# Kernel tuning notes

Measured on AMD Instinct MI355X. Metric: run time of the kernel, lower is better.

Reference implementation:

```python
import jax, jax.numpy as jnp
import numpy as np
from jax import lax

B, H, W = 8, 512, 512


def setup_inputs() -> dict:
    key = jax.random.key(0)
    k1, k2, k3, k4, k5 = jax.random.split(key, 5)
    img = jax.random.uniform(k1, (B, 3, H, W), jnp.float32)
    omega = 0.8 + 0.15 * jax.random.uniform(k2, (B, 1), jnp.float32)
    atmospheric_light = 0.5 + 0.5 * jax.random.uniform(k3, (B, 3), jnp.float32)
    L_low = 2.0 * jax.random.uniform(k4, (B, 1), jnp.float32)          # percent in [0,2)
    L_high = 95.0 + 4.0 * jax.random.uniform(k5, (B, 1), jnp.float32)  # percent in [95,99)
    guided_radius = 15  # python int, uniform across batch (original clamps to [1,50])
    return {"img": img, "omega": omega, "atmospheric_light": atmospheric_light,
            "L_low": L_low, "L_high": L_high, "guided_radius": guided_radius}


def _box_filter(x, r):
    # reflect-pad + mean over (2r+1)x(2r+1) window, separable (exactly avg_pool2d on reflect-padded input)
    k = 2 * r + 1
    xp = jnp.pad(x, ((0, 0), (0, 0), (r, r), (r, r)), mode='reflect')
    s = lax.reduce_window(xp, 0.0, lax.add, (1, 1, k, 1), (1, 1, 1, 1), 'VALID')
    s = lax.reduce_window(s, 0.0, lax.add, (1, 1, 1, k), (1, 1, 1, 1), 'VALID')
    return s / (k * k)


def _forward(img, omega, atmospheric_light, L_low, L_high, r):
    eps = 0.5
    Bb, Cc, Hh, Ww = img.shape
    A = atmospheric_light.reshape(Bb, 3, 1, 1)
    # initial transmission: t = 1 - omega * min_c(I/A)
    dark = jnp.min(img / (A + 1e-8), axis=1, keepdims=True)           # (B,1,H,W)
    t0 = 1.0 - omega.reshape(Bb, 1, 1, 1) * dark
    # gradient constraint (weights from t0, applied to shifted copies)
    wx = jnp.exp(-jnp.abs(t0[:, :, :, 1:] - t0[:, :, :, :-1]))
    tx = jnp.concatenate([t0[:, :, :, :1], t0[:, :, :, :-1] * wx], axis=3)
    wy = jnp.exp(-jnp.abs(t0[:, :, 1:, :] - t0[:, :, :-1, :]))
    tg = jnp.concatenate([tx[:, :, :1, :], tx[:, :, :-1, :] * wy], axis=2)
    # guided filter with grayscale guide
    rgb_w = jnp.array([0.299, 0.587, 0.114], dtype=img.dtype).reshape(1, 3, 1, 1)
    gray = jnp.sum(img * rgb_w, axis=1, keepdims=True)                # (B,1,H,W)
    mI = _box_filter(gray, r)
    mp = _box_filter(tg, r)
    mIp = _box_filter(gray * tg, r)
    cov_Ip = mIp - mI * mp
    var_I = _box_filter(gray * gray, r) - mI * mI
    a = cov_Ip / (var_I + eps)
    b = mp - a * mI
    t_final = jnp.clip(_box_filter(a, r) * gray + _box_filter(b, r), 0.1, 1.0)
    # restoration
    J = jnp.clip((img - A) / (t_final + 1e-8) + A, 0.0, 1.0)
    # percentile color stretch (vectorized over B and C)
    n = Hh * Ww
    svals = jnp.sort(J.reshape(Bb, Cc, n), axis=-1)
    li = jnp.clip((L_low / 100.0 * n).astype(jnp.int32), 0, n - 1)    # (B,1)
    hi = jnp.clip((L_high / 100.0 * n).astype(jnp.int32), 0, n - 1)
    p_low = jnp.take_along_axis(svals, jnp.broadcast_to(li[:, :, None], (Bb, Cc, 1)), axis=-1).reshape(Bb, Cc, 1, 1)
    p_high = jnp.take_along_axis(svals, jnp.broadcast_to(hi[:, :, None], (Bb, Cc, 1)), axis=-1).reshape(Bb, Cc, 1, 1)
    out = (jnp.clip(J, p_low, p_high) - p_low) / (p_high - p_low + 1e-8)
    return jnp.clip(out, 0.0, 1.0)


def reference(img, omega, atmospheric_light, L_low, L_high, guided_radius):
    r = max(1, min(int(guided_radius), 50))
    return _forward(img, omega, atmospheric_light, L_low, L_high, r)
```

## Files before the change

### kernel.cpp

```cpp
#include <hip/hip_runtime.h>
#include <cstdint>

constexpr int Bb = 8, Hh = 512, Ww = 512;
constexpr int HWn = Hh * Ww;
constexpr int CH23 = 16;
constexpr int CHK4 = 8;
constexpr int NBIN = 1024;
constexpr int NSUB = 32;

__device__ __forceinline__ int reflect_idx(int p, int n) {
    p = (p < 0) ? -p : p;
    return (p < n) ? p : (2 * n - 2 - p);
}
__device__ __forceinline__ int clamp_r(const int* rad) {
    int r = rad[0];
    return (r < 1) ? 1 : ((r > 50) ? 50 : r);
}

__global__ __launch_bounds__(512) void k1_stats_h(
    const float* __restrict__ img, const float* __restrict__ omega,
    const float* __restrict__ atm, const int* __restrict__ rad,
    float4* __restrict__ hq, unsigned int* __restrict__ histzero)
{
    const int i = blockIdx.x;
    const int b = blockIdx.y;
    const int j = threadIdx.x;
    const int fbid = b * gridDim.x + i;
    if (fbid < 48) histzero[fbid * 512 + j] = 0u;
    const int r = clamp_r(rad);

    __shared__ float t0c[512], t0p[512];
    __shared__ float4 Pb[512];
    __shared__ float4 wsum[8];

    const float om = omega[b];
    const float iA0 = 1.0f / (atm[b*3+0] + 1e-8f);
    const float iA1 = 1.0f / (atm[b*3+1] + 1e-8f);
    const float iA2 = 1.0f / (atm[b*3+2] + 1e-8f);
    const float* imb = img + (size_t)b * 3 * HWn;
    const int ip = (i > 0) ? (i - 1) : 0;

    float r0 = imb[0*HWn + i*Ww + j];
    float g0 = imb[1*HWn + i*Ww + j];
    float b0 = imb[2*HWn + i*Ww + j];
    t0c[j] = 1.0f - om * fminf(fminf(r0*iA0, g0*iA1), b0*iA2);
    float r1 = imb[0*HWn + ip*Ww + j];
    float g1 = imb[1*HWn + ip*Ww + j];
    float b1 = imb[2*HWn + ip*Ww + j];
    t0p[j] = 1.0f - om * fminf(fminf(r1*iA0, g1*iA1), b1*iA2);
    float gr = 0.299f*r0 + 0.587f*g0 + 0.114f*b0;
    __syncthreads();

    float tx = (j == 0) ? t0p[0] : t0p[j-1] * __expf(-fabsf(t0p[j] - t0p[j-1]));
    float tgv = (i == 0) ? tx : tx * __expf(-fabsf(t0c[j] - t0p[j]));

    const int lane = j & 63, wv = j >> 6;
    float4 incl;
    incl.x = gr; incl.y = tgv; incl.z = gr * tgv; incl.w = gr * gr;
    #pragma unroll
    for (int off = 1; off < 64; off <<= 1) {
        float ux = __shfl_up(incl.x, off);
        float uy = __shfl_up(incl.y, off);
        float uz = __shfl_up(incl.z, off);
        float uw = __shfl_up(incl.w, off);
        if (lane >= off) { incl.x += ux; incl.y += uy; incl.z += uz; incl.w += uw; }
    }
    if (lane == 63) wsum[wv] = incl;
    __syncthreads();
    float4 o4; o4.x = 0.f; o4.y = 0.f; o4.z = 0.f; o4.w = 0.f;
    #pragma unroll
    for (int w = 0; w < 7; ++w) {
        if (w < wv) {
            float4 t = wsum[w];
            o4.x += t.x; o4.y += t.y; o4.z += t.z; o4.w += t.w;
        }
    }
    float4 P; P.x = incl.x + o4.x; P.y = incl.y + o4.y; P.z = incl.z + o4.z; P.w = incl.w + o4.w;
    Pb[j] = P;
    __syncthreads();

    const int lo = j - r, hi = j + r;
    float4 s = Pb[(hi > 511) ? 511 : hi];
    if (lo > 0) {
        float4 t = Pb[lo-1];
        s.x -= t.x; s.y -= t.y; s.z -= t.z; s.w -= t.w;
    }
    if (lo < 0) {
        float4 t = Pb[r - j], u = Pb[0];
        s.x += t.x - u.x; s.y += t.y - u.y; s.z += t.z - u.z; s.w += t.w - u.w;
    }
    if (hi > 511) {
        float4 t = Pb[510], u = Pb[1021 - j - r];
        s.x += t.x - u.x; s.y += t.y - u.y; s.z += t.z - u.z; s.w += t.w - u.w;
    }
    hq[((size_t)b * Hh + i) * Ww + j] = s;
}

__global__ __launch_bounds__(512) void k23_ab_h(
    const float4* __restrict__ hq, const int* __restrict__ rad,
    float2* __restrict__ hab)
{
    const int b  = blockIdx.y;
    const int y0 = blockIdx.x * CH23;
    const int j  = threadIdx.x;
    const int r  = clamp_r(rad);
    const float ikk = 1.0f / (float)((2*r+1) * (2*r+1));
    const int lane = j & 63, wv = j >> 6;

    __shared__ float2 Pb8[CH23][512];
    __shared__ float2 wsum8[CH23][8];

    float4 s; s.x = 0.f; s.y = 0.f; s.z = 0.f; s.w = 0.f;
    for (int d = -r; d <= r; ++d) {
        int m = reflect_idx(y0 + d, Hh);
        float4 v = hq[((size_t)b * Hh + m) * Ww + j];
        s.x += v.x; s.y += v.y; s.z += v.z; s.w += v.w;
    }
    float av[CH23], bv[CH23];
    #pragma unroll
    for (int k = 0; k < CH23; ++k) {
        int y = y0 + k;
        float mI = s.x * ikk, mp = s.y * ikk, mIp = s.z * ikk, mII = s.w * ikk;
        float a = (mIp - mI * mp) / (mII - mI * mI + 0.5f);
        av[k] = a;
        bv[k] = mp - a * mI;
        int yin  = reflect_idx(y + 1 + r, Hh);
        int yout = reflect_idx(y - r, Hh);
        float4 vi = hq[((size_t)b * Hh + yin)  * Ww + j];
        float4 vo = hq[((size_t)b * Hh + yout) * Ww + j];
        s.x += vi.x - vo.x; s.y += vi.y - vo.y; s.z += vi.z - vo.z; s.w += vi.w - vo.w;
    }

    float ix[CH23], iy[CH23];
    #pragma unroll
    for (int k = 0; k < CH23; ++k) {
        float sx = av[k], sy = bv[k];
        #pragma unroll
        for (int off = 1; off < 64; off <<= 1) {
            float ux = __shfl_up(sx, off);
            float uy = __shfl_up(sy, off);
            if (lane >= off) { sx += ux; sy += uy; }
        }
        ix[k] = sx; iy[k] = sy;
        if (lane == 63) { wsum8[k][wv].x = sx; wsum8[k][wv].y = sy; }
    }
    __syncthreads();

    #pragma unroll
    for (int k = 0; k < CH23; ++k) {
        float ox = 0.f, oy = 0.f;
        #pragma unroll
        for (int w = 0; w < 7; ++w) {
            if (w < wv) { float2 t = wsum8[k][w]; ox += t.x; oy += t.y; }
        }
        Pb8[k][j].x = ix[k] + ox;
        Pb8[k][j].y = iy[k] + oy;
    }
    __syncthreads();

    const int lo = j - r, hi = j + r;
    const int him = (hi > 511) ? 511 : hi;
    #pragma unroll
    for (int k = 0; k < CH23; ++k) {
        float2 hs = Pb8[k][him];
        if (lo > 0)   { float2 t = Pb8[k][lo-1];  hs.x -= t.x; hs.y -= t.y; }
        if (lo < 0)   { float2 t = Pb8[k][r-j], u = Pb8[k][0];
                        hs.x += t.x - u.x; hs.y += t.y - u.y; }
        if (hi > 511) { float2 t = Pb8[k][510], u = Pb8[k][1021-j-r];
                        hs.x += t.x - u.x; hs.y += t.y - u.y; }
        hab[((size_t)b * Hh + (y0 + k)) * Ww + j] = hs;
    }
}

__global__ __launch_bounds__(128) void k4_final_v(
    const float4* __restrict__ hab4, const float4* __restrict__ img,
    const float* __restrict__ atm, const int* __restrict__ rad,
    float4* __restrict__ J)
{
    const int b  = blockIdx.y;
    const int y0 = blockIdx.x * CHK4;
    const int jc = threadIdx.x;
    const int r  = clamp_r(rad);
    const float ikk = 1.0f / (float)((2*r+1) * (2*r+1));
    const int HP = Ww / 2;
    const int CP = HWn / 4;
    const int RP = Ww / 4;

    float A0 = atm[b*3+0], A1 = atm[b*3+1], A2 = atm[b*3+2];
    const float4* imb  = img  + (size_t)b * 3 * CP;
    float4*       Jb   = J    + (size_t)b * 3 * CP;
    const float4* habb = hab4 + (size_t)b * Hh * HP + jc * 2;

    float2 V[4];
    #pragma unroll
    for (int q = 0; q < 4; ++q) { V[q].x = 0.f; V[q].y = 0.f; }
    for (int d = -r; d <= r; ++d) {
        int m = reflect_idx(y0 + d, Hh);
        float4 h0 = habb[(size_t)m * HP];
        float4 h1 = habb[(size_t)m * HP + 1];
        V[0].x += h0.x; V[0].y += h0.y;
        V[1].x += h0.z; V[1].y += h0.w;
        V[2].x += h1.x; V[2].y += h1.y;
        V[3].x += h1.z; V[3].y += h1.w;
    }

    for (int y = y0; y < y0 + CHK4; ++y) {
        const int yin  = reflect_idx(y + 1 + r, Hh);
        const int yout = reflect_idx(y - r, Hh);
        float4 i0 = habb[(size_t)yin  * HP];
        float4 i1 = habb[(size_t)yin  * HP + 1];
        float4 o0 = habb[(size_t)yout * HP];
        float4 o1 = habb[(size_t)yout * HP + 1];
        const size_t po = (size_t)y * RP + jc;
        float4 c0 = imb[0*CP + po];
        float4 c1 = imb[1*CP + po];
        float4 c2 = imb[2*CP + po];

        float cr[4] = {c0.x, c0.y, c0.z, c0.w};
        float cg[4] = {c1.x, c1.y, c1.z, c1.w};
        float cb[4] = {c2.x, c2.y, c2.z, c2.w};
        float o0v[4], o1v[4], o2v[4];
        #pragma unroll
        for (int q = 0; q < 4; ++q) {
            float g_ = 0.299f*cr[q] + 0.587f*cg[q] + 0.114f*cb[q];
            float t = fminf(fmaxf((V[q].x * g_ + V[q].y) * ikk, 0.1f), 1.0f);
            float invt = 1.0f / (t + 1e-8f);
            o0v[q] = fminf(fmaxf((cr[q] - A0) * invt + A0, 0.f), 1.f);
            o1v[q] = fminf(fmaxf((cg[q] - A1) * invt + A1, 0.f), 1.f);
            o2v[q] = fminf(fmaxf((cb[q] - A2) * invt + A2, 0.f), 1.f);
        }
        Jb[0*CP + po] = make_float4(o0v[0], o0v[1], o0v[2], o0v[3]);
        Jb[1*CP + po] = make_float4(o1v[0], o1v[1], o1v[2], o1v[3]);
        Jb[2*CP + po] = make_float4(o2v[0], o2v[1], o2v[2], o2v[3]);

        V[0].x += i0.x - o0.x; V[0].y += i0.y - o0.y;
        V[1].x += i0.z - o0.z; V[1].y += i0.w - o0.w;
        V[2].x += i1.x - o1.x; V[2].y += i1.y - o1.y;
        V[3].x += i1.z - o1.z; V[3].y += i1.w - o1.w;
    }
}

__global__ __launch_bounds__(256) void k5_hist(
    const float4* __restrict__ J, unsigned int* __restrict__ hist)
{
    const int bc  = blockIdx.x >> 5;
    const int sub = blockIdx.x & (NSUB - 1);
    const int tid = threadIdx.x;
    __shared__ unsigned int lh[NBIN];
    for (int i = tid; i < NBIN; i += 256) lh[i] = 0u;
    __syncthreads();

    const float4* base = J + (size_t)bc * (HWn / 4) + (size_t)sub * (HWn / 4 / NSUB);
    unsigned int clo = 0, chi = 0;
    for (int i = tid; i < HWn / 4 / NSUB; i += 256) {
        float4 v = base[i];
        #pragma unroll
        for (int c = 0; c < 4; ++c) {
            float f = (c == 0) ? v.x : (c == 1) ? v.y : (c == 2) ? v.z : v.w;
            int bin = (int)(f * (float)NBIN);
            bin = (bin > NBIN-1) ? NBIN-1 : bin;
            if (bin == 0)           clo++;
            else if (bin == NBIN-1) chi++;
            else atomicAdd(&lh[bin], 1u);
        }
    }
    if (clo) atomicAdd(&lh[0], clo);
    if (chi) atomicAdd(&lh[NBIN-1], chi);
    __syncthreads();
    for (int i = tid; i < NBIN; i += 256) {
        unsigned int v = lh[i];
        if (v) atomicAdd(&hist[(size_t)bc * NBIN + i], v);
    }
}

__global__ __launch_bounds__(64) void k5_decide(
    const unsigned int* __restrict__ hist,
    const float* __restrict__ L_low, const float* __restrict__ L_high,
    float* __restrict__ p_low, float* __restrict__ p_high)
{
    const int t  = blockIdx.x / 24;
    const int bc = blockIdx.x % 24;
    const int b  = bc / 3;
    const int lane = threadIdx.x;
    const unsigned int* hb = hist + (size_t)bc * NBIN;

    unsigned int loc[NBIN / 64];
    unsigned int lsum = 0;
    #pragma unroll
    for (int i = 0; i < NBIN / 64; ++i) { loc[i] = hb[lane * (NBIN/64) + i]; lsum += loc[i]; }

    unsigned int incl = lsum;
    #pragma unroll
    for (int off = 1; off < 64; off <<= 1) {
        unsigned int v = __shfl_up(incl, off);
        if (lane >= off) incl += v;
    }
    unsigned int excl = incl - lsum;

    float L = t ? L_high[b] : L_low[b];
    int k = (int)(L * (1.0f / 100.0f) * (float)HWn);
    k = (k < 0) ? 0 : ((k > HWn - 1) ? HWn - 1 : k);

    if ((unsigned int)k >= excl && (unsigned int)k < incl) {
        unsigned int c = excl;
        #pragma unroll
        for (int i = 0; i < NBIN / 64; ++i) {
            if ((unsigned int)k < c + loc[i]) {
                float val = ((float)(lane * (NBIN/64) + i) + 0.5f) * (1.0f / (float)NBIN);
                if (t) p_high[bc] = val;
                else   p_low[bc]  = val;
                break;
            }
            c += loc[i];
        }
    }
}

__global__ __launch_bounds__(256) void k6_norm(
    float4* __restrict__ J,
    const float* __restrict__ p_low, const float* __restrict__ p_high)
{
    size_t idx = (size_t)blockIdx.x * 256 + threadIdx.x;
    int bc = (int)(idx >> 16);
    float l = p_low[bc], h = p_high[bc];
    float inv = 1.0f / (h - l + 1e-8f);
    float4 v = J[idx];
    v.x = fminf(fmaxf((fminf(fmaxf(v.x, l), h) - l) * inv, 0.f), 1.f);
    v.y = fminf(fmaxf((fminf(fmaxf(v.y, l), h) - l) * inv, 0.f), 1.f);
    v.z = fminf(fmaxf((fminf(fmaxf(v.z, l), h) - l) * inv, 0.f), 1.f);
    v.w = fminf(fmaxf((fminf(fmaxf(v.w, l), h) - l) * inv, 0.f), 1.f);
    J[idx] = v;
}

extern "C" void kernel_launch(void* const* d_in, const int* in_sizes, int n_in,
                              void* d_out, int out_size, void* d_ws, size_t ws_size,
                              hipStream_t stream)
{
    const float* img    = (const float*)d_in[0];
    const float* omega  = (const float*)d_in[1];
    const float* atm    = (const float*)d_in[2];
    const float* L_low  = (const float*)d_in[3];
    const float* L_high = (const float*)d_in[4];
    const int*   rad    = (const int*)d_in[5];
    float* J  = (float*)d_out;
    float* ws = (float*)d_ws;

    const size_t F = (size_t)Bb * HWn;
    float4* hq  = (float4*)ws;
    float2* hab = (float2*)(ws + 4 * F);
    unsigned int* hist = (unsigned int*)(ws + 6 * F);
    float* pl = (float*)(hist + 24 * NBIN);
    float* ph = pl + 32;

    k1_stats_h<<<dim3(Hh, Bb), 512, 0, stream>>>(img, omega, atm, rad, hq, hist);
    k23_ab_h  <<<dim3(Hh/CH23, Bb), 512, 0, stream>>>(hq, rad, hab);
    k4_final_v<<<dim3(Hh/CHK4, Bb), 128, 0, stream>>>((const float4*)hab, (const float4*)img, atm, rad, (float4*)J);
    k5_hist   <<<24 * NSUB, 256, 0, stream>>>((const float4*)J, hist);
    k5_decide <<<48, 64, 0, stream>>>(hist, L_low, L_high, pl, ph);
    k6_norm   <<<(int)(3 * F / 4 / 256), 256, 0, stream>>>((float4*)J, pl, ph);
}
```

Measured before the change: 168.0 us.

## Fuse histogram into restoration kernel and percentile decision into normalize kernel

```diff
diff --git a/kernel.cpp b/kernel.cpp
--- a/kernel.cpp
+++ b/kernel.cpp
@@ -3,10 +3,10 @@
 
 constexpr int Bb = 8, Hh = 512, Ww = 512;
 constexpr int HWn = Hh * Ww;
+constexpr int CH1  = 8;
 constexpr int CH23 = 16;
 constexpr int CHK4 = 8;
 constexpr int NBIN = 1024;
-constexpr int NSUB = 32;
 
 __device__ __forceinline__ int reflect_idx(int p, int n) {
     p = (p < 0) ? -p : p;
@@ -22,14 +22,15 @@
     const float* __restrict__ atm, const int* __restrict__ rad,
     float4* __restrict__ hq, unsigned int* __restrict__ histzero)
 {
-    const int i = blockIdx.x;
+    const int tile = blockIdx.x;
     const int b = blockIdx.y;
+    const int y0 = tile * CH1;
     const int j = threadIdx.x;
-    const int fbid = b * gridDim.x + i;
+    const int fbid = b * gridDim.x + tile;
     if (fbid < 48) histzero[fbid * 512 + j] = 0u;
     const int r = clamp_r(rad);
 
-    __shared__ float t0c[512], t0p[512];
+    __shared__ float t0buf[2][512];
     __shared__ float4 Pb[512];
     __shared__ float4 wsum[8];
 
@@ -38,62 +39,72 @@
     const float iA1 = 1.0f / (atm[b*3+1] + 1e-8f);
     const float iA2 = 1.0f / (atm[b*3+2] + 1e-8f);
     const float* imb = img + (size_t)b * 3 * HWn;
-    const int ip = (i > 0) ? (i - 1) : 0;
-
-    float r0 = imb[0*HWn + i*Ww + j];
-    float g0 = imb[1*HWn + i*Ww + j];
-    float b0 = imb[2*HWn + i*Ww + j];
-    t0c[j] = 1.0f - om * fminf(fminf(r0*iA0, g0*iA1), b0*iA2);
-    float r1 = imb[0*HWn + ip*Ww + j];
-    float g1 = imb[1*HWn + ip*Ww + j];
-    float b1 = imb[2*HWn + ip*Ww + j];
-    t0p[j] = 1.0f - om * fminf(fminf(r1*iA0, g1*iA1), b1*iA2);
-    float gr = 0.299f*r0 + 0.587f*g0 + 0.114f*b0;
-    __syncthreads();
-
-    float tx = (j == 0) ? t0p[0] : t0p[j-1] * __expf(-fabsf(t0p[j] - t0p[j-1]));
-    float tgv = (i == 0) ? tx : tx * __expf(-fabsf(t0c[j] - t0p[j]));
+
+    {
+        const int yp = (y0 > 0) ? (y0 - 1) : 0;
+        float r1 = imb[0*HWn + yp*Ww + j];
+        float g1 = imb[1*HWn + yp*Ww + j];
+        float b1 = imb[2*HWn + yp*Ww + j];
+        t0buf[0][j] = 1.0f - om * fminf(fminf(r1*iA0, g1*iA1), b1*iA2);
+    }
+    __syncthreads();
 
     const int lane = j & 63, wv = j >> 6;
-    float4 incl;
-    incl.x = gr; incl.y = tgv; incl.z = gr * tgv; incl.w = gr * gr;
-    #pragma unroll
-    for (int off = 1; off < 64; off <<= 1) {
-        float ux = __shfl_up(incl.x, off);
-        float uy = __shfl_up(incl.y, off);
-        float uz = __shfl_up(incl.z, off);
-        float uw = __shfl_up(incl.w, off);
-        if (lane >= off) { incl.x += ux; incl.y += uy; incl.z += uz; incl.w += uw; }
-    }
-    if (lane == 63) wsum[wv] = incl;
-    __syncthreads();
-    float4 o4; o4.x = 0.f; o4.y = 0.f; o4.z = 0.f; o4.w = 0.f;
-    #pragma unroll
-    for (int w = 0; w < 7; ++w) {
-        if (w < wv) {
-            float4 t = wsum[w];
-            o4.x += t.x; o4.y += t.y; o4.z += t.z; o4.w += t.w;
-        }
-    }
-    float4 P; P.x = incl.x + o4.x; P.y = incl.y + o4.y; P.z = incl.z + o4.z; P.w = incl.w + o4.w;
-    Pb[j] = P;
-    __syncthreads();
-
-    const int lo = j - r, hi = j + r;
-    float4 s = Pb[(hi > 511) ? 511 : hi];
-    if (lo > 0) {
-        float4 t = Pb[lo-1];
-        s.x -= t.x; s.y -= t.y; s.z -= t.z; s.w -= t.w;
-    }
-    if (lo < 0) {
-        float4 t = Pb[r - j], u = Pb[0];
-        s.x += t.x - u.x; s.y += t.y - u.y; s.z += t.z - u.z; s.w += t.w - u.w;
-    }
-    if (hi > 511) {
-        float4 t = Pb[510], u = Pb[1021 - j - r];
-        s.x += t.x - u.x; s.y += t.y - u.y; s.z += t.z - u.z; s.w += t.w - u.w;
-    }
-    hq[((size_t)b * Hh + i) * Ww + j] = s;
+    int pv = 0;
+    for (int k = 0; k < CH1; ++k) {
+        const int y = y0 + k;
+        float r0 = imb[0*HWn + y*Ww + j];
+        float g0 = imb[1*HWn + y*Ww + j];
+        float b0 = imb[2*HWn + y*Ww + j];
+        float t0c = 1.0f - om * fminf(fminf(r0*iA0, g0*iA1), b0*iA2);
+        float gr = 0.299f*r0 + 0.587f*g0 + 0.114f*b0;
+        const float* t0p = t0buf[pv];
+        t0buf[pv^1][j] = t0c;
+        float tpj = t0p[j];
+        float tx  = (j == 0) ? t0p[0] : t0p[j-1] * __expf(-fabsf(tpj - t0p[j-1]));
+        float tgv = (y == 0) ? tx : tx * __expf(-fabsf(t0c - tpj));
+
+        float4 incl;
+        incl.x = gr; incl.y = tgv; incl.z = gr * tgv; incl.w = gr * gr;
+        #pragma unroll
+        for (int off = 1; off < 64; off <<= 1) {
+            float ux = __shfl_up(incl.x, off);
+            float uy = __shfl_up(incl.y, off);
+            float uz = __shfl_up(incl.z, off);
+            float uw = __shfl_up(incl.w, off);
+            if (lane >= off) { incl.x += ux; incl.y += uy; incl.z += uz; incl.w += uw; }
+        }
+        if (lane == 63) wsum[wv] = incl;
+        __syncthreads();
+        float4 o4; o4.x = 0.f; o4.y = 0.f; o4.z = 0.f; o4.w = 0.f;
+        #pragma unroll
+        for (int w = 0; w < 7; ++w) {
+            if (w < wv) {
+                float4 t = wsum[w];
+                o4.x += t.x; o4.y += t.y; o4.z += t.z; o4.w += t.w;
+            }
+        }
+        float4 P; P.x = incl.x + o4.x; P.y = incl.y + o4.y; P.z = incl.z + o4.z; P.w = incl.w + o4.w;
+        Pb[j] = P;
+        __syncthreads();
+
+        const int lo = j - r, hi = j + r;
+        float4 s = Pb[(hi > 511) ? 511 : hi];
+        if (lo > 0) {
+            float4 t = Pb[lo-1];
+            s.x -= t.x; s.y -= t.y; s.z -= t.z; s.w -= t.w;
+        }
+        if (lo < 0) {
+            float4 t = Pb[r - j], u = Pb[0];
+            s.x += t.x - u.x; s.y += t.y - u.y; s.z += t.z - u.z; s.w += t.w - u.w;
+        }
+        if (hi > 511) {
+            float4 t = Pb[510], u = Pb[1021 - j - r];
+            s.x += t.x - u.x; s.y += t.y - u.y; s.z += t.z - u.z; s.w += t.w - u.w;
+        }
+        hq[((size_t)b * Hh + y) * Ww + j] = s;
+        pv ^= 1;
+    }
 }
 
 __global__ __launch_bounds__(512) void k23_ab_h(
@@ -110,11 +121,21 @@
     __shared__ float2 Pb8[CH23][512];
     __shared__ float2 wsum8[CH23][8];
 
+    const float4* hqb = hq + (size_t)b * Hh * Ww + j;
     float4 s; s.x = 0.f; s.y = 0.f; s.z = 0.f; s.w = 0.f;
-    for (int d = -r; d <= r; ++d) {
-        int m = reflect_idx(y0 + d, Hh);
-        float4 v = hq[((size_t)b * Hh + m) * Ww + j];
-        s.x += v.x; s.y += v.y; s.z += v.z; s.w += v.w;
+    if (r == 15) {
+        #pragma unroll
+        for (int d = -15; d <= 15; ++d) {
+            int m = reflect_idx(y0 + d, Hh);
+            float4 v = hqb[(size_t)m * Ww];
+            s.x += v.x; s.y += v.y; s.z += v.z; s.w += v.w;
+        }
+    } else {
+        for (int d = -r; d <= r; ++d) {
+            int m = reflect_idx(y0 + d, Hh);
+            float4 v = hqb[(size_t)m * Ww];
+            s.x += v.x; s.y += v.y; s.z += v.z; s.w += v.w;
+        }
     }
     float av[CH23], bv[CH23];
     #pragma unroll
@@ -126,8 +147,8 @@
         bv[k] = mp - a * mI;
         int yin  = reflect_idx(y + 1 + r, Hh);
         int yout = reflect_idx(y - r, Hh);
-        float4 vi = hq[((size_t)b * Hh + yin)  * Ww + j];
-        float4 vo = hq[((size_t)b * Hh + yout) * Ww + j];
+        float4 vi = hqb[(size_t)yin  * Ww];
+        float4 vo = hqb[(size_t)yout * Ww];
         s.x += vi.x - vo.x; s.y += vi.y - vo.y; s.z += vi.z - vo.z; s.w += vi.w - vo.w;
     }
 
@@ -172,164 +193,166 @@
     }
 }
 
-__global__ __launch_bounds__(128) void k4_final_v(
-    const float4* __restrict__ hab4, const float4* __restrict__ img,
+__global__ __launch_bounds__(256) void k4_final_v(
+    const float4* __restrict__ hab4, const float2* __restrict__ img2,
     const float* __restrict__ atm, const int* __restrict__ rad,
-    float4* __restrict__ J)
-{
-    const int b  = blockIdx.y;
-    const int y0 = blockIdx.x * CHK4;
-    const int jc = threadIdx.x;
-    const int r  = clamp_r(rad);
+    float2* __restrict__ J2, unsigned int* __restrict__ hist)
+{
+    const int b   = blockIdx.y;
+    const int y0  = blockIdx.x * CHK4;
+    const int tid = threadIdx.x;
+    const int r   = clamp_r(rad);
     const float ikk = 1.0f / (float)((2*r+1) * (2*r+1));
-    const int HP = Ww / 2;
-    const int CP = HWn / 4;
-    const int RP = Ww / 4;
-
-    float A0 = atm[b*3+0], A1 = atm[b*3+1], A2 = atm[b*3+2];
-    const float4* imb  = img  + (size_t)b * 3 * CP;
-    float4*       Jb   = J    + (size_t)b * 3 * CP;
-    const float4* habb = hab4 + (size_t)b * Hh * HP + jc * 2;
-
-    float2 V[4];
-    #pragma unroll
-    for (int q = 0; q < 4; ++q) { V[q].x = 0.f; V[q].y = 0.f; }
-    for (int d = -r; d <= r; ++d) {
-        int m = reflect_idx(y0 + d, Hh);
-        float4 h0 = habb[(size_t)m * HP];
-        float4 h1 = habb[(size_t)m * HP + 1];
-        V[0].x += h0.x; V[0].y += h0.y;
-        V[1].x += h0.z; V[1].y += h0.w;
-        V[2].x += h1.x; V[2].y += h1.y;
-        V[3].x += h1.z; V[3].y += h1.w;
-    }
-
-    for (int y = y0; y < y0 + CHK4; ++y) {
+    const int HP4 = Ww / 2;
+    const int CP2 = HWn / 2;
+    const int RP2 = Ww / 2;
+
+    __shared__ unsigned int lh[3 * NBIN];
+    for (int i = tid; i < 3 * NBIN; i += 256) lh[i] = 0u;
+    __syncthreads();
+
+    const float A0 = atm[b*3+0], A1 = atm[b*3+1], A2 = atm[b*3+2];
+    const float2* imb = img2 + (size_t)b * 3 * CP2;
+    float2*       Jb  = J2   + (size_t)b * 3 * CP2;
+    const float4* habb = hab4 + (size_t)b * Hh * HP4 + tid;
+
+    float2 V0, V1;
+    V0.x = 0.f; V0.y = 0.f; V1.x = 0.f; V1.y = 0.f;
+    if (r == 15) {
+        #pragma unroll
+        for (int d = -15; d <= 15; ++d) {
+            int m = reflect_idx(y0 + d, Hh);
+            float4 h = habb[(size_t)m * HP4];
+            V0.x += h.x; V0.y += h.y; V1.x += h.z; V1.y += h.w;
+        }
+    } else {
+        for (int d = -r; d <= r; ++d) {
+            int m = reflect_idx(y0 + d, Hh);
+            float4 h = habb[(size_t)m * HP4];
+            V0.x += h.x; V0.y += h.y; V1.x += h.z; V1.y += h.w;
+        }
+    }
+
+    unsigned int clo0 = 0, chi0 = 0, clo1 = 0, chi1 = 0, clo2 = 0, chi2 = 0;
+
+    #pragma unroll
+    for (int k = 0; k < CHK4; ++k) {
+        const int y = y0 + k;
         const int yin  = reflect_idx(y + 1 + r, Hh);
         const int yout = reflect_idx(y - r, Hh);
-        float4 i0 = habb[(size_t)yin  * HP];
-        float4 i1 = habb[(size_t)yin  * HP + 1];
-        float4 o0 = habb[(size_t)yout * HP];
-        float4 o1 = habb[(size_t)yout * HP + 1];
-        const size_t po = (size_t)y * RP + jc;
-        float4 c0 = imb[0*CP + po];
-        float4 c1 = imb[1*CP + po];
-        float4 c2 = imb[2*CP + po];
-
-        float cr[4] = {c0.x, c0.y, c0.z, c0.w};
-        float cg[4] = {c1.x, c1.y, c1.z, c1.w};
-        float cb[4] = {c2.x, c2.y, c2.z, c2.w};
-        float o0v[4], o1v[4], o2v[4];
-        #pragma unroll
-        for (int q = 0; q < 4; ++q) {
-            float g_ = 0.299f*cr[q] + 0.587f*cg[q] + 0.114f*cb[q];
-            float t = fminf(fmaxf((V[q].x * g_ + V[q].y) * ikk, 0.1f), 1.0f);
-            float invt = 1.0f / (t + 1e-8f);
-            o0v[q] = fminf(fmaxf((cr[q] - A0) * invt + A0, 0.f), 1.f);
-            o1v[q] = fminf(fmaxf((cg[q] - A1) * invt + A1, 0.f), 1.f);
-            o2v[q] = fminf(fmaxf((cb[q] - A2) * invt + A2, 0.f), 1.f);
-        }
-        Jb[0*CP + po] = make_float4(o0v[0], o0v[1], o0v[2], o0v[3]);
-        Jb[1*CP + po] = make_float4(o1v[0], o1v[1], o1v[2], o1v[3]);
-        Jb[2*CP + po] = make_float4(o2v[0], o2v[1], o2v[2], o2v[3]);
-
-        V[0].x += i0.x - o0.x; V[0].y += i0.y - o0.y;
-        V[1].x += i0.z - o0.z; V[1].y += i0.w - o0.w;
-        V[2].x += i1.x - o1.x; V[2].y += i1.y - o1.y;
-        V[3].x += i1.z - o1.z; V[3].y += i1.w - o1.w;
-    }
-}
-
-__global__ __launch_bounds__(256) void k5_hist(
-    const float4* __restrict__ J, unsigned int* __restrict__ hist)
-{
-    const int bc  = blockIdx.x >> 5;
-    const int sub = blockIdx.x & (NSUB - 1);
-    const int tid = threadIdx.x;
-    __shared__ unsigned int lh[NBIN];
-    for (int i = tid; i < NBIN; i += 256) lh[i] = 0u;
-    __syncthreads();
-
-    const float4* base = J + (size_t)bc * (HWn / 4) + (size_t)sub * (HWn / 4 / NSUB);
-    unsigned int clo = 0, chi = 0;
-    for (int i = tid; i < HWn / 4 / NSUB; i += 256) {
-        float4 v = base[i];
-        #pragma unroll
-        for (int c = 0; c < 4; ++c) {
-            float f = (c == 0) ? v.x : (c == 1) ? v.y : (c == 2) ? v.z : v.w;
-            int bin = (int)(f * (float)NBIN);
-            bin = (bin > NBIN-1) ? NBIN-1 : bin;
-            if (bin == 0)           clo++;
-            else if (bin == NBIN-1) chi++;
-            else atomicAdd(&lh[bin], 1u);
-        }
-    }
-    if (clo) atomicAdd(&lh[0], clo);
-    if (chi) atomicAdd(&lh[NBIN-1], chi);
-    __syncthreads();
-    for (int i = tid; i < NBIN; i += 256) {
+        float4 hi4 = habb[(size_t)yin  * HP4];
+        float4 ho4 = habb[(size_t)yout * HP4];
+        const size_t po = (size_t)y * RP2 + tid;
+        float2 c0 = imb[0*CP2 + po];
+        float2 c1 = imb[1*CP2 + po];
+        float2 c2 = imb[2*CP2 + po];
+
+        float jr[2], jg[2], jb[2];
+        {
+            float g_ = 0.299f*c0.x + 0.587f*c1.x + 0.114f*c2.x;
+            float t  = fminf(fmaxf((V0.x * g_ + V0.y) * ikk, 0.1f), 1.0f);
+            float it = 1.0f / (t + 1e-8f);
+            jr[0] = fminf(fmaxf((c0.x - A0) * it + A0, 0.f), 1.f);
+            jg[0] = fminf(fmaxf((c1.x - A1) * it + A1, 0.f), 1.f);
+            jb[0] = fminf(fmaxf((c2.x - A2) * it + A2, 0.f), 1.f);
+        }
+        {
+            float g_ = 0.299f*c0.y + 0.587f*c1.y + 0.114f*c2.y;
+            float t  = fminf(fmaxf((V1.x * g_ + V1.y) * ikk, 0.1f), 1.0f);
+            float it = 1.0f / (t + 1e-8f);
+            jr[1] = fminf(fmaxf((c0.y - A0) * it + A0, 0.f), 1.f);
+            jg[1] = fminf(fmaxf((c1.y - A1) * it + A1, 0.f), 1.f);
+            jb[1] = fminf(fmaxf((c2.y - A2) * it + A2, 0.f), 1.f);
+        }
+        Jb[0*CP2 + po] = make_float2(jr[0], jr[1]);
+        Jb[1*CP2 + po] = make_float2(jg[0], jg[1]);
+        Jb[2*CP2 + po] = make_float2(jb[0], jb[1]);
+
+        #pragma unroll
+        for (int q = 0; q < 2; ++q) {
+            int bR = (int)(jr[q] * (float)NBIN); bR = (bR > NBIN-1) ? NBIN-1 : bR;
+            if (bR == 0) clo0++; else if (bR == NBIN-1) chi0++; else atomicAdd(&lh[0*NBIN + bR], 1u);
+            int bG = (int)(jg[q] * (float)NBIN); bG = (bG > NBIN-1) ? NBIN-1 : bG;
+            if (bG == 0) clo1++; else if (bG == NBIN-1) chi1++; else atomicAdd(&lh[1*NBIN + bG], 1u);
+            int bB = (int)(jb[q] * (float)NBIN); bB = (bB > NBIN-1) ? NBIN-1 : bB;
+            if (bB == 0) clo2++; else if (bB == NBIN-1) chi2++; else atomicAdd(&lh[2*NBIN + bB], 1u);
+        }
+
+        V0.x += hi4.x - ho4.x; V0.y += hi4.y - ho4.y;
+        V1.x += hi4.z - ho4.z; V1.y += hi4.w - ho4.w;
+    }
+
+    if (clo0) atomicAdd(&lh[0*NBIN],            clo0);
+    if (chi0) atomicAdd(&lh[0*NBIN + NBIN - 1], chi0);
+    if (clo1) atomicAdd(&lh[1*NBIN],            clo1);
+    if (chi1) atomicAdd(&lh[1*NBIN + NBIN - 1], chi1);
+    if (clo2) atomicAdd(&lh[2*NBIN],            clo2);
+    if (chi2) atomicAdd(&lh[2*NBIN + NBIN - 1], chi2);
+    __syncthreads();
+
+    const size_t hb = (size_t)b * 3 * NBIN;
+    for (int i = tid; i < 3 * NBIN; i += 256) {
         unsigned int v = lh[i];
-        if (v) atomicAdd(&hist[(size_t)bc * NBIN + i], v);
-    }
-}
-
-__global__ __launch_bounds__(64) void k5_decide(
-    const unsigned int* __restrict__ hist,
-    const float* __restrict__ L_low, const float* __restrict__ L_high,
-    float* __restrict__ p_low, float* __restrict__ p_high)
-{
-    const int t  = blockIdx.x / 24;
-    const int bc = blockIdx.x % 24;
-    const int b  = bc / 3;
-    const int lane = threadIdx.x;
-    const unsigned int* hb = hist + (size_t)bc * NBIN;
-
-    unsigned int loc[NBIN / 64];
-    unsigned int lsum = 0;
-    #pragma unroll
-    for (int i = 0; i < NBIN / 64; ++i) { loc[i] = hb[lane * (NBIN/64) + i]; lsum += loc[i]; }
-
-    unsigned int incl = lsum;
-    #pragma unroll
-    for (int off = 1; off < 64; off <<= 1) {
-        unsigned int v = __shfl_up(incl, off);
-        if (lane >= off) incl += v;
-    }
-    unsigned int excl = incl - lsum;
-
-    float L = t ? L_high[b] : L_low[b];
-    int k = (int)(L * (1.0f / 100.0f) * (float)HWn);
-    k = (k < 0) ? 0 : ((k > HWn - 1) ? HWn - 1 : k);
-
-    if ((unsigned int)k >= excl && (unsigned int)k < incl) {
-        unsigned int c = excl;
-        #pragma unroll
-        for (int i = 0; i < NBIN / 64; ++i) {
-            if ((unsigned int)k < c + loc[i]) {
-                float val = ((float)(lane * (NBIN/64) + i) + 0.5f) * (1.0f / (float)NBIN);
-                if (t) p_high[bc] = val;
-                else   p_low[bc]  = val;
-                break;
+        if (v) atomicAdd(&hist[hb + i], v);
+    }
+}
+
+__global__ __launch_bounds__(256) void k6_norm(
+    float4* __restrict__ J4, const unsigned int* __restrict__ hist,
+    const float* __restrict__ L_low, const float* __restrict__ L_high)
+{
+    const int bc  = blockIdx.x >> 6;
+    const int sub = blockIdx.x & 63;
+    const int b   = bc / 3;
+    __shared__ float sp[2];
+
+    if (threadIdx.x < 64) {
+        const int lane = threadIdx.x;
+        const unsigned int* hb = hist + (size_t)bc * NBIN;
+        unsigned int loc[NBIN / 64];
+        unsigned int lsum = 0;
+        #pragma unroll
+        for (int i = 0; i < NBIN / 64; ++i) { loc[i] = hb[lane * (NBIN/64) + i]; lsum += loc[i]; }
+        unsigned int incl = lsum;
+        #pragma unroll
+        for (int off = 1; off < 64; off <<= 1) {
+            unsigned int v = __shfl_up(incl, off);
+            if (lane >= off) incl += v;
+        }
+        unsigned int excl = incl - lsum;
+        #pragma unroll
+        for (int t = 0; t < 2; ++t) {
+            float L = t ? L_high[b] : L_low[b];
+            int k = (int)(L * (1.0f / 100.0f) * (float)HWn);
+            k = (k < 0) ? 0 : ((k > HWn - 1) ? HWn - 1 : k);
+            if ((unsigned int)k >= excl && (unsigned int)k < incl) {
+                unsigned int c = excl;
+                #pragma unroll
+                for (int i = 0; i < NBIN / 64; ++i) {
+                    if ((unsigned int)k < c + loc[i]) {
+                        sp[t] = ((float)(lane * (NBIN/64) + i) + 0.5f) * (1.0f / (float)NBIN);
+                        break;
+                    }
+                    c += loc[i];
+                }
             }
-            c += loc[i];
-        }
-    }
-}
-
-__global__ __launch_bounds__(256) void k6_norm(
-    float4* __restrict__ J,
-    const float* __restrict__ p_low, const float* __restrict__ p_high)
-{
-    size_t idx = (size_t)blockIdx.x * 256 + threadIdx.x;
-    int bc = (int)(idx >> 16);
-    float l = p_low[bc], h = p_high[bc];
-    float inv = 1.0f / (h - l + 1e-8f);
-    float4 v = J[idx];
-    v.x = fminf(fmaxf((fminf(fmaxf(v.x, l), h) - l) * inv, 0.f), 1.f);
-    v.y = fminf(fmaxf((fminf(fmaxf(v.y, l), h) - l) * inv, 0.f), 1.f);
-    v.z = fminf(fmaxf((fminf(fmaxf(v.z, l), h) - l) * inv, 0.f), 1.f);
-    v.w = fminf(fmaxf((fminf(fmaxf(v.w, l), h) - l) * inv, 0.f), 1.f);
-    J[idx] = v;
+        }
+    }
+    __syncthreads();
+
+    const float l = sp[0], h = sp[1];
+    const float inv = 1.0f / (h - l + 1e-8f);
+    float4* base = J4 + (size_t)bc * (HWn / 4) + (size_t)sub * 1024;
+    #pragma unroll
+    for (int s = 0; s < 4; ++s) {
+        const int idx = threadIdx.x + s * 256;
+        float4 v = base[idx];
+        v.x = fminf(fmaxf((fminf(fmaxf(v.x, l), h) - l) * inv, 0.f), 1.f);
+        v.y = fminf(fmaxf((fminf(fmaxf(v.y, l), h) - l) * inv, 0.f), 1.f);
+        v.z = fminf(fmaxf((fminf(fmaxf(v.z, l), h) - l) * inv, 0.f), 1.f);
+        v.w = fminf(fmaxf((fminf(fmaxf(v.w, l), h) - l) * inv, 0.f), 1.f);
+        base[idx] = v;
+    }
 }
 
 extern "C" void kernel_launch(void* const* d_in, const int* in_sizes, int n_in,
@@ -349,13 +372,9 @@
     float4* hq  = (float4*)ws;
     float2* hab = (float2*)(ws + 4 * F);
     unsigned int* hist = (unsigned int*)(ws + 6 * F);
-    float* pl = (float*)(hist + 24 * NBIN);
-    float* ph = pl + 32;
-
-    k1_stats_h<<<dim3(Hh, Bb), 512, 0, stream>>>(img, omega, atm, rad, hq, hist);
+
+    k1_stats_h<<<dim3(Hh/CH1,  Bb), 512, 0, stream>>>(img, omega, atm, rad, hq, hist);
     k23_ab_h  <<<dim3(Hh/CH23, Bb), 512, 0, stream>>>(hq, rad, hab);
-    k4_final_v<<<dim3(Hh/CHK4, Bb), 128, 0, stream>>>((const float4*)hab, (const float4*)img, atm, rad, (float4*)J);
-    k5_hist   <<<24 * NSUB, 256, 0, stream>>>((const float4*)J, hist);
-    k5_decide <<<48, 64, 0, stream>>>(hist, L_low, L_high, pl, ph);
-    k6_norm   <<<(int)(3 * F / 4 / 256), 256, 0, stream>>>((float4*)J, pl, ph);
-}
+    k4_final_v<<<dim3(Hh/CHK4, Bb), 256, 0, stream>>>((const float4*)hab, (const float2*)img, atm, rad, (float2*)J, hist);
+    k6_norm   <<<24 * 64, 256, 0, stream>>>((float4*)J, hist, L_low, L_high);
+}
```

After: 171.3 us. Within noise of the previous version (+2.0%).
